# Performance work log

Measured on AMD Instinct MI355X. Metric: run time of the kernel, lower is better.

The kernel has to match this reference:

```python
import jax, jax.numpy as jnp
import numpy as np

DIM = 1024
FF = 4096
BATCH = 4
SEQ = 2048
EPS = 1e-5


def setup_inputs() -> dict:
    key = jax.random.key(0)
    ks = jax.random.split(key, 8)
    x = jax.random.normal(ks[0], (BATCH, SEQ, DIM), dtype=jnp.float32)
    # phazor init: exp(2j*pi*arange(dim)/dim) * |randn(dim)|
    ang = 2.0 * np.pi * jnp.arange(DIM, dtype=jnp.float32) / DIM
    mag = jnp.abs(jax.random.normal(ks[1], (DIM,), dtype=jnp.float32))
    phazor_re = mag * jnp.cos(ang)
    phazor_im = mag * jnp.sin(ang)
    last_re = jax.random.normal(ks[2], (DIM,), dtype=jnp.float32)
    last_im = jax.random.normal(ks[3], (DIM,), dtype=jnp.float32)
    w1 = jax.random.normal(ks[4], (FF, DIM), dtype=jnp.float32) * DIM ** -0.5
    b1 = jnp.zeros((FF,), dtype=jnp.float32)
    w2 = jax.random.normal(ks[5], (DIM, FF), dtype=jnp.float32) * FF ** -0.5
    b2 = jnp.zeros((DIM,), dtype=jnp.float32)
    return {
        'x': x,
        'ln1_w': jnp.ones((DIM,), jnp.float32), 'ln1_b': jnp.zeros((DIM,), jnp.float32),
        'ln2_w': jnp.ones((DIM,), jnp.float32), 'ln2_b': jnp.zeros((DIM,), jnp.float32),
        'sc_lin': jnp.ones((DIM,), jnp.float32),
        'phazor_re': phazor_re, 'phazor_im': phazor_im,
        'last_re': last_re, 'last_im': last_im,
        'w1': w1, 'b1': b1, 'w2': w2, 'b2': b2,
    }


def _layer_norm(x, w, b):
    mu = jnp.mean(x, axis=-1, keepdims=True)
    var = jnp.mean(jnp.square(x - mu), axis=-1, keepdims=True)
    return (x - mu) * jax.lax.rsqrt(var + EPS) * w + b


def _sconv(x, phazor_re, phazor_im, last_re, last_im):
    B, L, D = x.shape
    dtype = x.dtype
    xc = x.astype(jnp.complex64)
    p_raw = phazor_re + 1j * phazor_im
    # tanh(|p|) * exp(i*angle(p))
    p = (jnp.tanh(jnp.abs(p_raw)) * jnp.exp(1j * jnp.angle(p_raw))).astype(jnp.complex64)
    t = jnp.arange(L)[:, None]
    prog = jnp.power(p[None, :], t)            # [L, D] complex
    filt_fft = jnp.fft.fft(prog, n=2 * L, axis=0)   # [2L, D]
    x_fft = jnp.fft.fft(xc, n=2 * L, axis=1)        # [B, 2L, D]
    conv = jnp.fft.ifft(filt_fft[None] * x_fft, axis=1)[:, :L]  # [B, L, D]
    last = (last_re + 1j * last_im)[None, None, :]  # [1,1,D] broadcast over batch
    conv_with_past = conv + last * prog[None] * p[None, None]
    return conv_with_past.real.astype(dtype)


def reference(x, ln1_w, ln1_b, ln2_w, ln2_b, sc_lin,
              phazor_re, phazor_im, last_re, last_im,
              w1, b1, w2, b2):
    # SConv branch
    x_res = x
    h = _layer_norm(x, ln1_w, ln1_b)
    h = jax.nn.silu(h)
    h = _sconv(h, phazor_re, phazor_im, last_re, last_im)
    h = h * sc_lin
    x = h + x_res
    # FFN branch
    x_res = x
    h = _layer_norm(x, ln2_w, ln2_b)
    h = jax.nn.silu(jnp.einsum('bld,fd->blf', h, w1) + b1)
    h = jnp.einsum('blf,df->bld', h, w2) + b2
    return h + x_res
```

## Files before the change

### kernel.cpp

```cpp
#include <hip/hip_runtime.h>
#include <cmath>


#define DIMD 1024
#define FFD  4096
#define BATCH 4
#define SEQL 2048
#define MROWS (BATCH*SEQL)
#define EPSF 1e-5f
#define CHUNKS 32
#define CLEN (SEQL/CHUNKS)

typedef __attribute__((ext_vector_type(8))) _Float16 half8;
typedef __attribute__((ext_vector_type(4))) _Float16 half4;
typedef __attribute__((ext_vector_type(4))) float    floatx4;

#define H_OFF    0u
#define E_OFF    33554432u
#define SIN_OFF  34603008u
#define H2_OFF   35651584u
#define W1H_OFF  52428800u
#define W2H_OFF  60817408u
#define Y1_OFF   69206016u

__device__ __forceinline__ void load_lds16(const _Float16* g, _Float16* l) {
    __builtin_amdgcn_global_load_lds(
        (const __attribute__((address_space(1))) unsigned int*)g,
        (__attribute__((address_space(3))) unsigned int*)l,
        16, 0, 0);
}

__global__ __launch_bounds__(256)
void cast_f32_f16(const float* __restrict__ src, _Float16* __restrict__ dst) {
    int i = (blockIdx.x * 256 + threadIdx.x) * 4;
    float4 v = *(const float4*)(src + i);
    half4 o;
    o.x = (_Float16)v.x; o.y = (_Float16)v.y; o.z = (_Float16)v.z; o.w = (_Float16)v.w;
    *(half4*)(dst + i) = o;
}

__global__ __launch_bounds__(256)
void ln_kernel(const float* __restrict__ x, const float* __restrict__ w,
               const float* __restrict__ b, float* __restrict__ of,
               _Float16* __restrict__ oh, int mode) {
    const size_t row = blockIdx.x;
    const int tid = threadIdx.x;
    float4 v = *(const float4*)(x + row * DIMD + tid * 4);
    float s = (v.x + v.y) + (v.z + v.w);
    float q = (v.x * v.x + v.y * v.y) + (v.z * v.z + v.w * v.w);
    #pragma unroll
    for (int off = 32; off; off >>= 1) {
        s += __shfl_down(s, off, 64);
        q += __shfl_down(q, off, 64);
    }
    __shared__ float red[8];
    if (!(tid & 63)) { red[tid >> 6] = s; red[4 + (tid >> 6)] = q; }
    __syncthreads();
    s = (red[0] + red[1]) + (red[2] + red[3]);
    q = (red[4] + red[5]) + (red[6] + red[7]);
    const float mu = s * (1.f / DIMD);
    const float rs = rsqrtf(q * (1.f / DIMD) - mu * mu + EPSF);
    float4 wv = *(const float4*)(w + tid * 4);
    float4 bv = *(const float4*)(b + tid * 4);
    float o0 = (v.x - mu) * rs * wv.x + bv.x;
    float o1 = (v.y - mu) * rs * wv.y + bv.y;
    float o2 = (v.z - mu) * rs * wv.z + bv.z;
    float o3 = (v.w - mu) * rs * wv.w + bv.w;
    if (mode == 1) {
        o0 = o0 / (1.f + __expf(-o0));
        o1 = o1 / (1.f + __expf(-o1));
        o2 = o2 / (1.f + __expf(-o2));
        o3 = o3 / (1.f + __expf(-o3));
        float4 ov = {o0, o1, o2, o3};
        *(float4*)(of + row * DIMD + tid * 4) = ov;
    } else {
        half4 hv;
        hv.x = (_Float16)o0; hv.y = (_Float16)o1;
        hv.z = (_Float16)o2; hv.w = (_Float16)o3;
        *(half4*)(oh + row * DIMD + tid * 4) = hv;
    }
}

__device__ __forceinline__ void get_p(const float* pre, const float* pim, int d,
                                      float& pr, float& pi) {
    float re = pre[d], im = pim[d];
    float r = sqrtf(re * re + im * im);
    float t = tanhf(r) / fmaxf(r, 1e-30f);
    pr = re * t; pi = im * t;
}

__global__ __launch_bounds__(256)
void scan_partial(const float* __restrict__ h, const float* __restrict__ pre,
                  const float* __restrict__ pim, float2* __restrict__ e) {
    const int d = blockIdx.x * 256 + threadIdx.x;
    const int c = blockIdx.y;
    const int bb = blockIdx.z;
    float pr, pi; get_p(pre, pim, d, pr, pi);
    float sr = 0.f, si = 0.f;
    const float* hp = h + ((size_t)bb * SEQL + (size_t)c * CLEN) * DIMD + d;
    #pragma unroll 4
    for (int j = 0; j < CLEN; ++j) {
        float hv = hp[(size_t)j * DIMD];
        float nr = pr * sr - pi * si + hv;
        float ni = pr * si + pi * sr;
        sr = nr; si = ni;
    }
    e[((size_t)bb * CHUNKS + c) * DIMD + d] = make_float2(sr, si);
}

__global__ __launch_bounds__(256)
void scan_combine(const float2* __restrict__ e, const float* __restrict__ pre,
                  const float* __restrict__ pim, const float* __restrict__ lre,
                  const float* __restrict__ lim, float2* __restrict__ sv) {
    const int d = blockIdx.x * 256 + threadIdx.x;
    const int bb = blockIdx.y;
    float pr, pi; get_p(pre, pim, d, pr, pi);
    float qr = pr, qi = pi;
    #pragma unroll
    for (int s = 0; s < 6; ++s) {
        float nr = qr * qr - qi * qi;
        float ni = 2.f * qr * qi;
        qr = nr; qi = ni;
    }
    float sr = lre[d], si = lim[d];
    for (int c = 0; c < CHUNKS; ++c) {
        sv[((size_t)bb * CHUNKS + c) * DIMD + d] = make_float2(sr, si);
        float2 ec = e[((size_t)bb * CHUNKS + c) * DIMD + d];
        float nr = qr * sr - qi * si + ec.x;
        float ni = qr * si + qi * sr + ec.y;
        sr = nr; si = ni;
    }
}

__global__ __launch_bounds__(256)
void scan_final(const float* __restrict__ h, const float* __restrict__ x,
                const float* __restrict__ pre, const float* __restrict__ pim,
                const float* __restrict__ sc, const float2* __restrict__ sv,
                float* __restrict__ x2) {
    const int d = blockIdx.x * 256 + threadIdx.x;
    const int c = blockIdx.y;
    const int bb = blockIdx.z;
    float pr, pi; get_p(pre, pim, d, pr, pi);
    float2 s0 = sv[((size_t)bb * CHUNKS + c) * DIMD + d];
    float sr = s0.x, si = s0.y;
    const float scd = sc[d];
    const size_t base = ((size_t)bb * SEQL + (size_t)c * CLEN) * DIMD + d;
    #pragma unroll 4
    for (int j = 0; j < CLEN; ++j) {
        float hv = h[base + (size_t)j * DIMD];
        float nr = pr * sr - pi * si + hv;
        float ni = pr * si + pi * sr;
        sr = nr; si = ni;
        x2[base + (size_t)j * DIMD] = x[base + (size_t)j * DIMD] + scd * sr;
    }
}

#define MEMF asm volatile("" ::: "memory")
#define BARR do { MEMF; __builtin_amdgcn_s_barrier(); MEMF; } while (0)

template<int BN, int WM, int WN, int EPI>
__global__ __launch_bounds__(512)
void gemm8p(const _Float16* __restrict__ A, const _Float16* __restrict__ W,
            const float* __restrict__ bias, _Float16* __restrict__ out_h,
            const float* resid, float* out_f, int N, int K) {
    constexpr int BM = 256, BK = 64;
    constexpr int RC = (BM / 2) / WM;
    constexpr int CC = (BN / 2) / WN;
    constexpr int FR = RC / 16;
    constexpr int FC = CC / 16;
    constexpr int BI = BN / 128;

    __shared__ __align__(16) _Float16 As[2 * BM * BK];
    __shared__ __align__(16) _Float16 Bs[2 * BN * BK];

    const int tid  = threadIdx.x;
    const int lane = tid & 63;
    const int wave = tid >> 6;
    const int fr   = lane & 15;
    const int quad = lane >> 4;
    const int wm   = wave / WN;
    const int wn   = wave % WN;

    const int nx  = N / BN;
    const int nwg = nx * (MROWS / BM);
    const int lb  = blockIdx.y * gridDim.x + blockIdx.x;
    const int sid = (lb & 7) * (nwg >> 3) + (lb >> 3);
    const size_t m0 = (size_t)(sid / nx) * BM;
    const size_t n0 = (size_t)(sid % nx) * BN;

    const int srow = lane >> 3;
    const int gch  = (lane & 7) ^ srow;
    const _Float16* Ag = A + (m0 + (size_t)(wave * 8 + srow)) * K + gch * 8;
    const _Float16* Wg = W + (n0 + (size_t)(wave * 8 + srow)) * K + gch * 8;
    _Float16* Asl = &As[(wave * 8) * BK];
    _Float16* Bsl = &Bs[(wave * 8) * BK];

#define STAGE_A(b, kt, h) do { \
    load_lds16(Ag + (size_t)((h)*128 +  0) * K + (size_t)(kt) * BK, \
               Asl + ((b)*BM + (h)*128 +  0) * BK); \
    load_lds16(Ag + (size_t)((h)*128 + 64) * K + (size_t)(kt) * BK, \
               Asl + ((b)*BM + (h)*128 + 64) * BK); \
} while (0)

#define STAGE_B(b, kt, h) do { \
    load_lds16(Wg + (size_t)((h)*(BN/2) +  0) * K + (size_t)(kt) * BK, \
               Bsl + ((b)*BN + (h)*(BN/2) +  0) * BK); \
    if (BI == 2) \
    load_lds16(Wg + (size_t)((h)*(BN/2) + 64) * K + (size_t)(kt) * BK, \
               Bsl + ((b)*BN + (h)*(BN/2) + 64) * BK); \
} while (0)

    half8 Af[FR][2], Bf[FC][2];

#define READ_A(b, rg) do { \
    _Pragma("unroll") \
    for (int f_ = 0; f_ < FR; ++f_) { \
        const int R_ = (rg)*128 + wm*RC + f_*16 + fr; \
        _Pragma("unroll") \
        for (int ks_ = 0; ks_ < 2; ++ks_) { \
            const int slot_ = (ks_*4 + quad) ^ (fr & 7); \
            Af[f_][ks_] = *(const half8*)&As[((b)*BM + R_) * BK + slot_*8]; \
        } \
    } \
} while (0)

#define READ_B(b, cg) do { \
    _Pragma("unroll") \
    for (int j_ = 0; j_ < FC; ++j_) { \
        const int Rb_ = (cg)*(BN/2) + wn*CC + j_*16 + fr; \
        _Pragma("unroll") \
        for (int ks_ = 0; ks_ < 2; ++ks_) { \
            const int slot_ = (ks_*4 + quad) ^ (fr & 7); \
            Bf[j_][ks_] = *(const half8*)&Bs[((b)*BN + Rb_) * BK + slot_*8]; \
        } \
    } \
} while (0)

#define MM(rg, cg) do { \
    _Pragma("unroll") \
    for (int f_ = 0; f_ < FR; ++f_) \
    _Pragma("unroll") \
    for (int j_ = 0; j_ < FC; ++j_) \
    _Pragma("unroll") \
    for (int ks_ = 0; ks_ < 2; ++ks_) \
        acc[(rg)*FR + f_][(cg)*FC + j_] = __builtin_amdgcn_mfma_f32_16x16x32_f16( \
            Af[f_][ks_], Bf[j_][ks_], acc[(rg)*FR + f_][(cg)*FC + j_], 0, 0, 0); \
} while (0)

#define WAIT_STEADY do { \
    if constexpr (BN == 256) asm volatile("s_waitcnt vmcnt(6)" ::: "memory"); \
    else                     asm volatile("s_waitcnt vmcnt(5)" ::: "memory"); \
} while (0)

    floatx4 acc[2 * FR][2 * FC] = {};
    const int nt = K / BK;

    STAGE_A(0, 0, 0);
    STAGE_A(0, 0, 1);
    STAGE_B(0, 0, 0);
    STAGE_B(0, 0, 1);
    STAGE_A(1, 1, 0);
    STAGE_B(1, 1, 1);
    STAGE_A(1, 1, 1);
    WAIT_STEADY;
    BARR;

    for (int t = 0; t < nt; ++t) {
        const int cur = t & 1;
        const int nxt = cur ^ 1;
        READ_A(cur, 0);
        READ_B(cur, 0);
        if (t + 1 < nt) STAGE_B(nxt, t + 1, 0);
        BARR;
        __builtin_amdgcn_s_setprio(1); MM(0, 0); __builtin_amdgcn_s_setprio(0);
        BARR;
        READ_B(cur, 1);
        if (t + 2 < nt) STAGE_A(cur, t + 2, 0);
        BARR;
        __builtin_amdgcn_s_setprio(1); MM(0, 1); __builtin_amdgcn_s_setprio(0);
        BARR;
        READ_A(cur, 1);
        if (t + 2 < nt) STAGE_B(cur, t + 2, 1);
        BARR;
        __builtin_amdgcn_s_setprio(1); MM(1, 1); __builtin_amdgcn_s_setprio(0);
        BARR;
        READ_B(cur, 0);
        if (t + 2 < nt) STAGE_A(cur, t + 2, 1);
        BARR;
        __builtin_amdgcn_s_setprio(1); MM(1, 0); __builtin_amdgcn_s_setprio(0);
        if (t < nt - 2) WAIT_STEADY;
        else            asm volatile("s_waitcnt vmcnt(0)" ::: "memory");
        BARR;
    }

    #pragma unroll
    for (int rg = 0; rg < 2; ++rg)
    #pragma unroll
    for (int f = 0; f < FR; ++f)
    #pragma unroll
    for (int cg = 0; cg < 2; ++cg)
    #pragma unroll
    for (int j = 0; j < FC; ++j) {
        const floatx4 a = acc[rg * FR + f][cg * FC + j];
        const size_t gn = n0 + cg * (BN / 2) + wn * CC + j * 16 + fr;
        const float bb = bias[gn];
        #pragma unroll
        for (int r = 0; r < 4; ++r) {
            const size_t gm = m0 + rg * 128 + wm * RC + f * 16 + quad * 4 + r;
            float v = a[r] + bb;
            if (EPI == 1) {
                float sl = v / (1.f + __expf(-v));
                out_h[gm * (size_t)N + gn] = (_Float16)sl;
            } else {
                out_f[gm * (size_t)N + gn] = v + resid[gm * (size_t)N + gn];
            }
        }
    }
#undef STAGE_A
#undef STAGE_B
#undef READ_A
#undef READ_B
#undef MM
#undef WAIT_STEADY
}

extern "C" void kernel_launch(void* const* d_in, const int* in_sizes, int n_in,
                              void* d_out, int out_size, void* d_ws, size_t ws_size,
                              hipStream_t stream) {
    const float* x    = (const float*)d_in[0];
    const float* ln1w = (const float*)d_in[1];
    const float* ln1b = (const float*)d_in[2];
    const float* ln2w = (const float*)d_in[3];
    const float* ln2b = (const float*)d_in[4];
    const float* sc   = (const float*)d_in[5];
    const float* pre  = (const float*)d_in[6];
    const float* pim  = (const float*)d_in[7];
    const float* lre  = (const float*)d_in[8];
    const float* lim  = (const float*)d_in[9];
    const float* w1   = (const float*)d_in[10];
    const float* b1   = (const float*)d_in[11];
    const float* w2   = (const float*)d_in[12];
    const float* b2   = (const float*)d_in[13];

    char* ws = (char*)d_ws;
    float*      h   = (float*)(ws + H_OFF);
    float2*     e   = (float2*)(ws + E_OFF);
    float2*     sv  = (float2*)(ws + SIN_OFF);
    _Float16*   h2  = (_Float16*)(ws + H2_OFF);
    _Float16*   w1h = (_Float16*)(ws + W1H_OFF);
    _Float16*   w2h = (_Float16*)(ws + W2H_OFF);
    _Float16*   y1  = (_Float16*)(ws + Y1_OFF);
    float*      x2  = (float*)d_out;
    float*      outp = (float*)d_out;

    cast_f32_f16<<<dim3(FFD * DIMD / 1024), 256, 0, stream>>>(w1, w1h);
    cast_f32_f16<<<dim3(FFD * DIMD / 1024), 256, 0, stream>>>(w2, w2h);
    ln_kernel<<<dim3(MROWS), 256, 0, stream>>>(x, ln1w, ln1b, h, nullptr, 1);
    scan_partial<<<dim3(DIMD / 256, CHUNKS, BATCH), 256, 0, stream>>>(h, pre, pim, e);
    scan_combine<<<dim3(DIMD / 256, BATCH), 256, 0, stream>>>(e, pre, pim, lre, lim, sv);
    scan_final<<<dim3(DIMD / 256, CHUNKS, BATCH), 256, 0, stream>>>(h, x, pre, pim, sc, sv, x2);
    ln_kernel<<<dim3(MROWS), 256, 0, stream>>>(x2, ln2w, ln2b, nullptr, h2, 2);
    gemm8p<256, 2, 4, 1><<<dim3(FFD / 256, MROWS / 256), 512, 0, stream>>>(
        h2, w1h, b1, y1, nullptr, nullptr, FFD, DIMD);
    gemm8p<128, 4, 2, 2><<<dim3(DIMD / 128, MROWS / 256), 512, 0, stream>>>(
        y1, w2h, b2, nullptr, x2, outp, DIMD, FFD);
}
```

Measured before the change: 361.8 us.

## Fuse LN1+SiLU into scan kernels via row stats; replace second GEMM

The first layernorm now writes only per-row mean and rstd. The normalize and SiLU step is recomputed inside scan_partial and scan_final from x, so the 32 MB fp32 intermediate h is never written or read back. The second FFN GEMM also switches from the 256x128 pipelined gemm8p to a simpler 128x128 tile kernel with a single LDS buffer and grouped block ordering. That kernel has no multi-stage pipelining, so it may stall on loads, and the LN+SiLU work is now computed twice.

```diff
diff --git a/kernel.cpp b/kernel.cpp
--- a/kernel.cpp
+++ b/kernel.cpp
@@ -15,7 +15,7 @@
 typedef __attribute__((ext_vector_type(4))) _Float16 half4;
 typedef __attribute__((ext_vector_type(4))) float    floatx4;
 
-#define H_OFF    0u
+#define ST_OFF   0u
 #define E_OFF    33554432u
 #define SIN_OFF  34603008u
 #define H2_OFF   35651584u
@@ -40,9 +40,32 @@
 }
 
 __global__ __launch_bounds__(256)
+void ln_stats(const float* __restrict__ x, float2* __restrict__ st) {
+    const size_t row = blockIdx.x;
+    const int tid = threadIdx.x;
+    float4 v = *(const float4*)(x + row * DIMD + tid * 4);
+    float s = (v.x + v.y) + (v.z + v.w);
+    float q = (v.x * v.x + v.y * v.y) + (v.z * v.z + v.w * v.w);
+    #pragma unroll
+    for (int off = 32; off; off >>= 1) {
+        s += __shfl_down(s, off, 64);
+        q += __shfl_down(q, off, 64);
+    }
+    __shared__ float red[8];
+    if (!(tid & 63)) { red[tid >> 6] = s; red[4 + (tid >> 6)] = q; }
+    __syncthreads();
+    if (tid == 0) {
+        s = (red[0] + red[1]) + (red[2] + red[3]);
+        q = (red[4] + red[5]) + (red[6] + red[7]);
+        const float mu = s * (1.f / DIMD);
+        const float rs = rsqrtf(q * (1.f / DIMD) - mu * mu + EPSF);
+        st[row] = make_float2(mu, rs);
+    }
+}
+
+__global__ __launch_bounds__(256)
 void ln_kernel(const float* __restrict__ x, const float* __restrict__ w,
-               const float* __restrict__ b, float* __restrict__ of,
-               _Float16* __restrict__ oh, int mode) {
+               const float* __restrict__ b, _Float16* __restrict__ oh) {
     const size_t row = blockIdx.x;
     const int tid = threadIdx.x;
     float4 v = *(const float4*)(x + row * DIMD + tid * 4);
@@ -62,23 +85,12 @@
     const float rs = rsqrtf(q * (1.f / DIMD) - mu * mu + EPSF);
     float4 wv = *(const float4*)(w + tid * 4);
     float4 bv = *(const float4*)(b + tid * 4);
-    float o0 = (v.x - mu) * rs * wv.x + bv.x;
-    float o1 = (v.y - mu) * rs * wv.y + bv.y;
-    float o2 = (v.z - mu) * rs * wv.z + bv.z;
-    float o3 = (v.w - mu) * rs * wv.w + bv.w;
-    if (mode == 1) {
-        o0 = o0 / (1.f + __expf(-o0));
-        o1 = o1 / (1.f + __expf(-o1));
-        o2 = o2 / (1.f + __expf(-o2));
-        o3 = o3 / (1.f + __expf(-o3));
-        float4 ov = {o0, o1, o2, o3};
-        *(float4*)(of + row * DIMD + tid * 4) = ov;
-    } else {
-        half4 hv;
-        hv.x = (_Float16)o0; hv.y = (_Float16)o1;
-        hv.z = (_Float16)o2; hv.w = (_Float16)o3;
-        *(half4*)(oh + row * DIMD + tid * 4) = hv;
-    }
+    half4 hv;
+    hv.x = (_Float16)((v.x - mu) * rs * wv.x + bv.x);
+    hv.y = (_Float16)((v.y - mu) * rs * wv.y + bv.y);
+    hv.z = (_Float16)((v.z - mu) * rs * wv.z + bv.z);
+    hv.w = (_Float16)((v.w - mu) * rs * wv.w + bv.w);
+    *(half4*)(oh + row * DIMD + tid * 4) = hv;
 }
 
 __device__ __forceinline__ void get_p(const float* pre, const float* pim, int d,
@@ -89,18 +101,28 @@
     pr = re * t; pi = im * t;
 }
 
-__global__ __launch_bounds__(256)
-void scan_partial(const float* __restrict__ h, const float* __restrict__ pre,
-                  const float* __restrict__ pim, float2* __restrict__ e) {
+__device__ __forceinline__ float ln_silu(float xv, float2 st, float wd, float bd) {
+    float o = (xv - st.x) * st.y * wd + bd;
+    return o / (1.f + __expf(-o));
+}
+
+__global__ __launch_bounds__(256)
+void scan_partial(const float* __restrict__ x, const float2* __restrict__ st,
+                  const float* __restrict__ lw, const float* __restrict__ lb,
+                  const float* __restrict__ pre, const float* __restrict__ pim,
+                  float2* __restrict__ e) {
     const int d = blockIdx.x * 256 + threadIdx.x;
     const int c = blockIdx.y;
     const int bb = blockIdx.z;
     float pr, pi; get_p(pre, pim, d, pr, pi);
+    const float wd = lw[d], bd = lb[d];
     float sr = 0.f, si = 0.f;
-    const float* hp = h + ((size_t)bb * SEQL + (size_t)c * CLEN) * DIMD + d;
+    const size_t row0 = (size_t)bb * SEQL + (size_t)c * CLEN;
     #pragma unroll 4
     for (int j = 0; j < CLEN; ++j) {
-        float hv = hp[(size_t)j * DIMD];
+        float xv = x[(row0 + j) * DIMD + d];
+        float2 sj = st[row0 + j];
+        float hv = ln_silu(xv, sj, wd, bd);
         float nr = pr * sr - pi * si + hv;
         float ni = pr * si + pi * sr;
         sr = nr; si = ni;
@@ -133,7 +155,8 @@
 }
 
 __global__ __launch_bounds__(256)
-void scan_final(const float* __restrict__ h, const float* __restrict__ x,
+void scan_final(const float* __restrict__ x, const float2* __restrict__ st,
+                const float* __restrict__ lw, const float* __restrict__ lb,
                 const float* __restrict__ pre, const float* __restrict__ pim,
                 const float* __restrict__ sc, const float2* __restrict__ sv,
                 float* __restrict__ x2) {
@@ -141,17 +164,20 @@
     const int c = blockIdx.y;
     const int bb = blockIdx.z;
     float pr, pi; get_p(pre, pim, d, pr, pi);
+    const float wd = lw[d], bd = lb[d];
     float2 s0 = sv[((size_t)bb * CHUNKS + c) * DIMD + d];
     float sr = s0.x, si = s0.y;
     const float scd = sc[d];
-    const size_t base = ((size_t)bb * SEQL + (size_t)c * CLEN) * DIMD + d;
+    const size_t row0 = (size_t)bb * SEQL + (size_t)c * CLEN;
     #pragma unroll 4
     for (int j = 0; j < CLEN; ++j) {
-        float hv = h[base + (size_t)j * DIMD];
+        float xv = x[(row0 + j) * DIMD + d];
+        float2 sj = st[row0 + j];
+        float hv = ln_silu(xv, sj, wd, bd);
         float nr = pr * sr - pi * si + hv;
         float ni = pr * si + pi * sr;
         sr = nr; si = ni;
-        x2[base + (size_t)j * DIMD] = x[base + (size_t)j * DIMD] + scd * sr;
+        x2[(row0 + j) * DIMD + d] = xv + scd * sr;
     }
 }
 
@@ -322,6 +348,78 @@
 #undef READ_B
 #undef MM
 #undef WAIT_STEADY
+}
+
+#define G2BM 128
+#define G2BN 128
+#define G2BK 64
+
+__global__ __launch_bounds__(256)
+void gemm2_128(const _Float16* __restrict__ A, const _Float16* __restrict__ W,
+               const float* __restrict__ bias, const float* __restrict__ resid,
+               float* __restrict__ out_f, int N, int K) {
+    __shared__ _Float16 As[G2BM * G2BK];
+    __shared__ _Float16 Bs[G2BN * G2BK];
+    const int tid  = threadIdx.x;
+    const int lane = tid & 63;
+    const int wave = tid >> 6;
+    const int wm = (wave >> 1) * 64;
+    const int wn = (wave & 1) * 64;
+    const int n  = blockIdx.y * gridDim.x + blockIdx.x;
+    const int xc = n & 7, ii = n >> 3;
+    const size_t m0 = (size_t)(xc + ((ii >> 3) << 3)) * G2BM;
+    const size_t n0 = (size_t)(ii & 7) * G2BN;
+    const int fr = lane & 15;
+    const int quad = lane >> 4;
+
+    const int srow = wave * 32 + (lane >> 3);
+    const int ccp  = ((lane & 7) ^ (lane >> 3)) * 8;
+    const _Float16* ag = A + (m0 + srow) * (size_t)K + ccp;
+    const _Float16* wg = W + (n0 + srow) * (size_t)K + ccp;
+    _Float16* asl = &As[(wave * 32) * G2BK];
+    _Float16* bsl = &Bs[(wave * 32) * G2BK];
+
+    floatx4 acc[4][4] = {};
+
+    for (int k0 = 0; k0 < K; k0 += G2BK) {
+        #pragma unroll
+        for (int t = 0; t < 4; ++t) {
+            load_lds16(ag + k0 + (size_t)(t * 8) * K, asl + t * 8 * G2BK);
+            load_lds16(wg + k0 + (size_t)(t * 8) * K, bsl + t * 8 * G2BK);
+        }
+        __syncthreads();
+        #pragma unroll
+        for (int kk = 0; kk < G2BK; kk += 32) {
+            half8 af[4], bf[4];
+            #pragma unroll
+            for (int i = 0; i < 4; ++i) {
+                const int slot = (((kk >> 3) + quad) ^ (fr & 7)) * 8;
+                af[i] = *(const half8*)(&As[(wm + i * 16 + fr) * G2BK + slot]);
+                bf[i] = *(const half8*)(&Bs[(wn + i * 16 + fr) * G2BK + slot]);
+            }
+            #pragma unroll
+            for (int i = 0; i < 4; ++i)
+                #pragma unroll
+                for (int j = 0; j < 4; ++j)
+                    acc[i][j] = __builtin_amdgcn_mfma_f32_16x16x32_f16(
+                        af[i], bf[j], acc[i][j], 0, 0, 0);
+        }
+        __syncthreads();
+    }
+
+    #pragma unroll
+    for (int i = 0; i < 4; ++i) {
+        #pragma unroll
+        for (int j = 0; j < 4; ++j) {
+            #pragma unroll
+            for (int r = 0; r < 4; ++r) {
+                const size_t gm = m0 + wm + i * 16 + quad * 4 + r;
+                const size_t gn = n0 + wn + j * 16 + fr;
+                float v = acc[i][j][r] + bias[gn];
+                out_f[gm * N + gn] = v + resid[gm * N + gn];
+            }
+        }
+    }
 }
 
 extern "C" void kernel_launch(void* const* d_in, const int* in_sizes, int n_in,
@@ -343,7 +441,7 @@
     const float* b2   = (const float*)d_in[13];
 
     char* ws = (char*)d_ws;
-    float*      h   = (float*)(ws + H_OFF);
+    float2*     st  = (float2*)(ws + ST_OFF);
     float2*     e   = (float2*)(ws + E_OFF);
     float2*     sv  = (float2*)(ws + SIN_OFF);
     _Float16*   h2  = (_Float16*)(ws + H2_OFF);
@@ -355,13 +453,15 @@
 
     cast_f32_f16<<<dim3(FFD * DIMD / 1024), 256, 0, stream>>>(w1, w1h);
     cast_f32_f16<<<dim3(FFD * DIMD / 1024), 256, 0, stream>>>(w2, w2h);
-    ln_kernel<<<dim3(MROWS), 256, 0, stream>>>(x, ln1w, ln1b, h, nullptr, 1);
-    scan_partial<<<dim3(DIMD / 256, CHUNKS, BATCH), 256, 0, stream>>>(h, pre, pim, e);
+    ln_stats<<<dim3(MROWS), 256, 0, stream>>>(x, st);
+    scan_partial<<<dim3(DIMD / 256, CHUNKS, BATCH), 256, 0, stream>>>(
+        x, st, ln1w, ln1b, pre, pim, e);
     scan_combine<<<dim3(DIMD / 256, BATCH), 256, 0, stream>>>(e, pre, pim, lre, lim, sv);
-    scan_final<<<dim3(DIMD / 256, CHUNKS, BATCH), 256, 0, stream>>>(h, x, pre, pim, sc, sv, x2);
-    ln_kernel<<<dim3(MROWS), 256, 0, stream>>>(x2, ln2w, ln2b, nullptr, h2, 2);
+    scan_final<<<dim3(DIMD / 256, CHUNKS, BATCH), 256, 0, stream>>>(
+        x, st, ln1w, ln1b, pre, pim, sc, sv, x2);
+    ln_kernel<<<dim3(MROWS), 256, 0, stream>>>(x2, ln2w, ln2b, h2);
     gemm8p<256, 2, 4, 1><<<dim3(FFD / 256, MROWS / 256), 512, 0, stream>>>(
         h2, w1h, b1, y1, nullptr, nullptr, FFD, DIMD);
-    gemm8p<128, 4, 2, 2><<<dim3(DIMD / 128, MROWS / 256), 512, 0, stream>>>(
-        y1, w2h, b2, nullptr, x2, outp, DIMD, FFD);
-}
+    gemm2_128<<<dim3(DIMD / G2BN, MROWS / G2BM), 256, 0, stream>>>(
+        y1, w2h, b2, x2, outp, DIMD, FFD);
+}
```

Result: faster. 345.2 us (-4.6%).
